# Kernel optimization log

Hardware: AMD Instinct MI355X
Metric: run time of the kernel (lower is better)

## Reference

```python
import jax, jax.numpy as jnp
import numpy as np

B, S, H = 32, 64, 512
ATT = 128


def _window_index_tables(seq_len):
    # Enumerate all contiguous windows of size 2..S, same set (order-independent
    # for the softmax-weighted sum) as the torch double loop.
    starts, ends = [], []
    for w in range(2, seq_len + 1):
        for s in range(0, seq_len - w + 1):
            starts.append(s)
            ends.append(s + w)
    starts = np.asarray(starts, np.int32)
    ends = np.asarray(ends, np.int32)
    widths = ends - starts
    ks = np.floor(np.log2(widths)).astype(np.int32)  # sparse-table level per window
    e2 = ends - (1 << ks)                            # second gather position
    return starts, e2, ks


def setup_inputs() -> dict:
    key = jax.random.key(0)
    k0, k1, k2, k3, k4 = jax.random.split(key, 5)
    return {
        "lstm_out": jax.random.normal(k0, (B, S, H), dtype=jnp.float32),
        "W1": jax.random.normal(k1, (H, ATT), dtype=jnp.float32) * 0.05,
        "b1": jax.random.normal(k2, (ATT,), dtype=jnp.float32) * 0.05,
        "W2": jax.random.normal(k3, (ATT, 1), dtype=jnp.float32) * 0.05,
        "b2": jax.random.normal(k4, (1,), dtype=jnp.float32) * 0.05,
    }


def reference(lstm_out, W1, b1, W2, b2):
    b, s, h = lstm_out.shape
    # Sparse table: M[k][:, i] = max over lstm_out[:, i : i+2^k] (clipped to s).
    n_levels = int(np.floor(np.log2(s))) + 1
    tables = [lstm_out]
    for k in range(1, n_levels):
        half = 1 << (k - 1)
        prev = tables[-1]
        shifted = jnp.concatenate(
            [prev[:, half:], jnp.full((b, half, h), -jnp.inf, prev.dtype)], axis=1)
        tables.append(jnp.maximum(prev, shifted))
    Mstack = jnp.stack(tables)  # [K, B, S, H]

    starts, e2, ks = _window_index_tables(s)
    # Range max of each window = max of two overlapping power-of-two blocks.
    pooled = jnp.maximum(Mstack[ks, :, starts], Mstack[ks, :, e2])  # [n_win, B, H]
    pooled = jnp.transpose(pooled, (1, 0, 2))  # [B, n_win, H]

    hid = jax.nn.relu(jnp.einsum("bnh,ha->bna", pooled, W1) + b1)
    scores = jnp.einsum("bna,ao->bno", hid, W2) + b2  # [B, n_win, 1]
    attn = jax.nn.softmax(scores, axis=1)
    return jnp.sum(attn * pooled, axis=1)  # [B, H]
```

## Files before the change

### kernel.cpp

```cpp
#include <hip/hip_runtime.h>
#include <stdint.h>


typedef unsigned short u16;
typedef unsigned int u32;

#define B_    32
#define S_    64
#define H_    512
#define ATT_  128
#define NWIN  2016
#define NLEV  7

typedef __bf16 bf16x8 __attribute__((ext_vector_type(8)));
typedef float  f32x4  __attribute__((ext_vector_type(4)));

__device__ __forceinline__ float asf(u32 i) {
  union { u32 i; float f; } v; v.i = i; return v.f;
}
__device__ __forceinline__ u32 asu(float f) {
  union { float f; u32 i; } v; v.f = f; return v.i;
}
__device__ __forceinline__ float bf2f(u16 u) { return asf(((u32)u) << 16); }
__device__ __forceinline__ u16 f2bf(float f) {
  u32 i = asu(f);
  i += 0x7fffu + ((i >> 16) & 1u);
  return (u16)(i >> 16);
}
__device__ __forceinline__ u32 bfmax2(u32 a, u32 b) {
  float a0 = asf(a << 16), a1 = asf(a & 0xffff0000u);
  float b0 = asf(b << 16), b1 = asf(b & 0xffff0000u);
  u32 m0 = asu(fmaxf(a0, b0)), m1 = asu(fmaxf(a1, b1));
  return (m1 & 0xffff0000u) | (m0 >> 16);
}
__device__ __forceinline__ uint4 bfmax8(uint4 a, uint4 b) {
  uint4 m;
  m.x = bfmax2(a.x, b.x); m.y = bfmax2(a.y, b.y);
  m.z = bfmax2(a.z, b.z); m.w = bfmax2(a.w, b.w);
  return m;
}
__device__ __forceinline__ bf16x8 as_bf16x8(uint4 v) {
  union { uint4 u; bf16x8 h; } c; c.u = v; return c.h;
}

__launch_bounds__(256)
__global__ void k01_init(const float* __restrict__ lstm, const float* __restrict__ W1,
                         u16* __restrict__ table, u16* __restrict__ w1t,
                         u16* __restrict__ widx) {
  int bid = blockIdx.x, tid = threadIdx.x;
  __shared__ u16 bufA[64 * 64], bufB[64 * 64];
  if (bid < 256) {
    int hc = bid & 7, b = bid >> 3;
    const float* src = lstm + (size_t)b * S_ * H_ + hc * 64;
    u16* tb = table + (size_t)b * NLEV * S_ * H_ + hc * 64;
    for (int t = tid; t < 64 * 16; t += 256) {
      int r = t >> 4, c4 = t & 15;
      float4 f = *reinterpret_cast<const float4*>(src + r * H_ + c4 * 4);
      ushort4 u;
      u.x = f2bf(f.x); u.y = f2bf(f.y); u.z = f2bf(f.z); u.w = f2bf(f.w);
      *reinterpret_cast<ushort4*>(&bufA[r * 64 + c4 * 4]) = u;
      *reinterpret_cast<ushort4*>(tb + r * H_ + c4 * 4) = u;
    }
    u16* pa = bufA; u16* pb = bufB;
    for (int k = 1; k < NLEV; ++k) {
      __syncthreads();
      int half = 1 << (k - 1);
      u16* dst_g = tb + k * S_ * H_;
      for (int t = tid; t < 64 * 16; t += 256) {
        int r = t >> 4, c4 = t & 15;
        int r2 = r + half; if (r2 > 63) r2 = 63;
        uint2 a  = *reinterpret_cast<const uint2*>(&pa[r  * 64 + c4 * 4]);
        uint2 bq = *reinterpret_cast<const uint2*>(&pa[r2 * 64 + c4 * 4]);
        uint2 m; m.x = bfmax2(a.x, bq.x); m.y = bfmax2(a.y, bq.y);
        *reinterpret_cast<uint2*>(&pb[r * 64 + c4 * 4]) = m;
        *reinterpret_cast<uint2*>(dst_g + r * H_ + c4 * 4) = m;
      }
      u16* tmp = pa; pa = pb; pb = tmp;
    }
  } else {
    int gb = bid - 256;
    if (gb == 0) {
      for (int n = tid; n < NWIN; n += 256) {
        int w = 2, rem = n;
        while (rem >= 65 - w) { rem -= 65 - w; ++w; }
        int s = rem;
        int k = 31 - __clz(w);
        int e2 = s + w - (1 << k);
        widx[n] = (u16)(s | (e2 << 6) | (k << 12));
      }
    }
    for (int q = tid; q < 2048; q += 256) {
      int idx = gb * 2048 + q;
      int n = idx >> 9, kq = idx & 511;
      w1t[idx] = f2bf(W1[kq * ATT_ + n]);
    }
  }
}

__launch_bounds__(256)
__attribute__((amdgpu_waves_per_eu(1, 4)))
__global__ void k2_scores(const u16* __restrict__ table, const u16* __restrict__ w1t,
                          const float* __restrict__ b1, const float* __restrict__ w2,
                          const u16* __restrict__ widx, float* __restrict__ scores) {
  const int b = blockIdx.y, mt = blockIdx.x;
  __shared__ u16 Ts[128 * 64];
  __shared__ u16 Bs[128 * 64];
  __shared__ u16 widx_l[96];
  __shared__ float b1s[128], w2s[128], sc[96];
  int tid = threadIdx.x;
  if (tid < 96) { widx_l[tid] = widx[mt * 96 + tid]; sc[tid] = 0.f; }
  if (tid < 128) { b1s[tid] = b1[tid]; w2s[tid] = w2[tid]; }
  __syncthreads();

  const int lv_lo = widx_l[0] >> 12;
  const u16* tb = table + (size_t)b * NLEV * S_ * H_ + (size_t)lv_lo * S_ * H_;

  int t0 = tid, t1 = tid + 256, t2 = tid + 512, t3 = tid + 768;
  int r0 = t0 >> 3, r1 = t1 >> 3, r2 = t2 >> 3, r3 = t3 >> 3;
  int c0 = t0 & 7,  c1 = t1 & 7,  c2 = t2 & 7,  c3 = t3 & 7;
  const u16* ts0 = tb + r0 * H_ + c0 * 8;
  const u16* ts1 = tb + r1 * H_ + c1 * 8;
  const u16* ts2 = tb + r2 * H_ + c2 * 8;
  const u16* ts3 = tb + r3 * H_ + c3 * 8;
  const u16* bs0 = w1t + r0 * H_ + c0 * 8;
  const u16* bs1 = w1t + r1 * H_ + c1 * 8;
  const u16* bs2 = w1t + r2 * H_ + c2 * 8;
  const u16* bs3 = w1t + r3 * H_ + c3 * 8;
  int sd0 = r0 * 64 + ((c0 ^ (r0 & 7)) * 8);
  int sd1 = r1 * 64 + ((c1 ^ (r1 & 7)) * 8);
  int sd2 = r2 * 64 + ((c2 ^ (r2 & 7)) * 8);
  int sd3 = r3 * 64 + ((c3 ^ (r3 & 7)) * 8);

  int wid = tid >> 6, lane = tid & 63;
  int wm = wid & 1, wn = wid >> 1;
  int lrow = lane & 15, quad = lane >> 4;

  int aoff[3][2][2];
#pragma unroll
  for (int i = 0; i < 3; ++i) {
    int m = wm * 48 + i * 16 + lrow;
    int pk = widx_l[m];
    int s = pk & 63, e2 = (pk >> 6) & 63, lv = (pk >> 12) - lv_lo;
    int rs = lv * 64 + s, re = lv * 64 + e2;
#pragma unroll
    for (int k2i = 0; k2i < 2; ++k2i) {
      int c = quad + k2i * 4;
      aoff[i][k2i][0] = rs * 64 + ((c ^ (rs & 7)) * 8);
      aoff[i][k2i][1] = re * 64 + ((c ^ (re & 7)) * 8);
    }
  }
  int boff[4][2];
#pragma unroll
  for (int j = 0; j < 4; ++j) {
    int n = wn * 64 + j * 16 + lrow;
#pragma unroll
    for (int k2i = 0; k2i < 2; ++k2i) {
      int c = quad + k2i * 4;
      boff[j][k2i] = n * 64 + ((c ^ (n & 7)) * 8);
    }
  }

  uint4 rT0, rT1, rT2, rT3, rB0, rB1, rB2, rB3;

#define ISSUE(KK) do { \
  rT0 = *reinterpret_cast<const uint4*>(ts0 + (KK)); \
  rT1 = *reinterpret_cast<const uint4*>(ts1 + (KK)); \
  rT2 = *reinterpret_cast<const uint4*>(ts2 + (KK)); \
  rT3 = *reinterpret_cast<const uint4*>(ts3 + (KK)); \
  rB0 = *reinterpret_cast<const uint4*>(bs0 + (KK)); \
  rB1 = *reinterpret_cast<const uint4*>(bs1 + (KK)); \
  rB2 = *reinterpret_cast<const uint4*>(bs2 + (KK)); \
  rB3 = *reinterpret_cast<const uint4*>(bs3 + (KK)); \
} while (0)

#define STAGE() do { \
  *reinterpret_cast<uint4*>(&Ts[sd0]) = rT0; \
  *reinterpret_cast<uint4*>(&Ts[sd1]) = rT1; \
  *reinterpret_cast<uint4*>(&Ts[sd2]) = rT2; \
  *reinterpret_cast<uint4*>(&Ts[sd3]) = rT3; \
  *reinterpret_cast<uint4*>(&Bs[sd0]) = rB0; \
  *reinterpret_cast<uint4*>(&Bs[sd1]) = rB1; \
  *reinterpret_cast<uint4*>(&Bs[sd2]) = rB2; \
  *reinterpret_cast<uint4*>(&Bs[sd3]) = rB3; \
} while (0)

#define MFMA_CHUNK() do { \
  _Pragma("unroll") for (int k2i = 0; k2i < 2; ++k2i) { \
    bf16x8 af[3], bfr[4]; \
    _Pragma("unroll") for (int i = 0; i < 3; ++i) { \
      uint4 va = *reinterpret_cast<const uint4*>(&Ts[aoff[i][k2i][0]]); \
      uint4 vb = *reinterpret_cast<const uint4*>(&Ts[aoff[i][k2i][1]]); \
      af[i] = as_bf16x8(bfmax8(va, vb)); } \
    _Pragma("unroll") for (int j = 0; j < 4; ++j) \
      bfr[j] = *reinterpret_cast<const bf16x8*>(&Bs[boff[j][k2i]]); \
    _Pragma("unroll") for (int i = 0; i < 3; ++i) \
      _Pragma("unroll") for (int j = 0; j < 4; ++j) \
        acc[i][j] = __builtin_amdgcn_mfma_f32_16x16x32_bf16(af[i], bfr[j], acc[i][j], 0, 0, 0); \
  } \
} while (0)

  ISSUE(0);

  f32x4 acc[3][4];
#pragma unroll
  for (int i = 0; i < 3; ++i)
#pragma unroll
    for (int j = 0; j < 4; ++j) acc[i][j] = (f32x4){0.f, 0.f, 0.f, 0.f};

  for (int kc = 0; kc < 7; ++kc) {
    __syncthreads();
    STAGE();
    __syncthreads();
    ISSUE((kc + 1) * 64);
    MFMA_CHUNK();
  }
  __syncthreads();
  STAGE();
  __syncthreads();
  MFMA_CHUNK();

#undef ISSUE
#undef STAGE
#undef MFMA_CHUNK

#pragma unroll
  for (int i = 0; i < 3; ++i) {
#pragma unroll
    for (int r = 0; r < 4; ++r) {
      float p = 0.f;
#pragma unroll
      for (int j = 0; j < 4; ++j) {
        int n = wn * 64 + j * 16 + lrow;
        float v = acc[i][j][r] + b1s[n];
        p += (v > 0.f ? v : 0.f) * w2s[n];
      }
      p += __shfl_xor(p, 1, 16);
      p += __shfl_xor(p, 2, 16);
      p += __shfl_xor(p, 4, 16);
      p += __shfl_xor(p, 8, 16);
      if (lrow == 0) atomicAdd(&sc[wm * 48 + i * 16 + quad * 4 + r], p);
    }
  }
  __syncthreads();
  if (tid < 96) scores[b * NWIN + mt * 96 + tid] = sc[tid];
}

__launch_bounds__(256)
__global__ void k34_out(const u16* __restrict__ table, const float* __restrict__ scores,
                        const u16* __restrict__ widx, float* __restrict__ out) {
  int hc = blockIdx.x, b = blockIdx.y, tid = threadIdx.x;
  __shared__ u16 Tl[6 * 64 * 32];
  __shared__ float attn_l[NWIN];
  __shared__ u16 widx_l[NWIN];
  __shared__ float red[8][32];
  __shared__ float wredM[4], wredS[4];
  const u16* tb = table + (size_t)b * NLEV * S_ * H_ + S_ * H_;
  int h0 = hc * 32;
  int lane = tid & 63, wid = tid >> 6;

  for (int t = tid; t < 6 * 64 * 4; t += 256) {
    int row = t >> 2, c = t & 3;
    uint4 v = *reinterpret_cast<const uint4*>(tb + row * H_ + h0 + c * 8);
    *reinterpret_cast<uint4*>(&Tl[row * 32 + c * 8]) = v;
  }
  for (int n = tid; n < NWIN; n += 256) widx_l[n] = widx[n];

  float mx = -1e30f;
  for (int n = tid; n < NWIN; n += 256) {
    float v = scores[b * NWIN + n];
    attn_l[n] = v;
    mx = fmaxf(mx, v);
  }
#pragma unroll
  for (int off = 32; off > 0; off >>= 1) mx = fmaxf(mx, __shfl_xor(mx, off, 64));
  if (lane == 0) wredM[wid] = mx;
  __syncthreads();
  mx = fmaxf(fmaxf(wredM[0], wredM[1]), fmaxf(wredM[2], wredM[3]));
  float sum = 0.f;
  for (int n = tid; n < NWIN; n += 256) {
    float e = __expf(attn_l[n] - mx);
    attn_l[n] = e;
    sum += e;
  }
#pragma unroll
  for (int off = 32; off > 0; off >>= 1) sum += __shfl_xor(sum, off, 64);
  if (lane == 0) wredS[wid] = sum;
  __syncthreads();
  float inv = 1.f / (wredS[0] + wredS[1] + wredS[2] + wredS[3]);

  int h = tid & 31, g = tid >> 5;
  float acc = 0.f;
  for (int n = g * 252; n < g * 252 + 252; ++n) {
    int pk = widx_l[n];
    int s = pk & 63, e2 = (pk >> 6) & 63, lv = pk >> 12;
    float va = bf2f(Tl[((lv - 1) * 64 + s) * 32 + h]);
    float vb = bf2f(Tl[((lv - 1) * 64 + e2) * 32 + h]);
    acc += attn_l[n] * fmaxf(va, vb);
  }
  red[g][h] = acc;
  __syncthreads();
  if (tid < 32) {
    float s2 = 0.f;
#pragma unroll
    for (int g2 = 0; g2 < 8; ++g2) s2 += red[g2][tid];
    out[b * H_ + h0 + tid] = s2 * inv;
  }
}

extern "C" void kernel_launch(void* const* d_in, const int* in_sizes, int n_in,
                              void* d_out, int out_size, void* d_ws, size_t ws_size,
                              hipStream_t stream) {
  const float* lstm = (const float*)d_in[0];
  const float* W1   = (const float*)d_in[1];
  const float* b1   = (const float*)d_in[2];
  const float* W2   = (const float*)d_in[3];
  float* out = (float*)d_out;

  char* ws = (char*)d_ws;
  u16*   widx   = (u16*)(ws + 0);
  u16*   w1t    = (u16*)(ws + 4096);
  u16*   table  = (u16*)(ws + 135168);
  float* scores = (float*)(ws + 14815232);

  k01_init <<<288, 256, 0, stream>>>(lstm, W1, table, w1t, widx);
  k2_scores<<<dim3(21, B_), 256, 0, stream>>>(table, w1t, b1, W2, widx, scores);
  k34_out  <<<dim3(16, B_), 256, 0, stream>>>(table, scores, widx, out);
}
```

Before: 123.8 us.

## Retile score GEMM to 64-window tiles and drop unused level-0 table

The score kernel now gives each block 64 windows instead of 96. Each wave handles 16 windows across all 128 attention columns, so the shared-memory atomic reduction is gone and scores are written directly. The grid grows from 21 to 32 tiles per batch, and the last tile is partially masked. The sparse table no longer stores level 0, since windows start at width 2. This saves global writes and workspace, and all table indexing is shifted by one level. The cost is that each block still stages the same full 128-row tile for fewer windows, so the redundant staged loads grow.

Measured after the change: 116.6 us. 1.06x faster.

```diff
diff --git a/kernel.cpp b/kernel.cpp
--- a/kernel.cpp
+++ b/kernel.cpp
@@ -11,6 +11,7 @@
 #define ATT_  128
 #define NWIN  2016
 #define NLEV  7
+#define TLEV  6
 
 typedef __bf16 bf16x8 __attribute__((ext_vector_type(8)));
 typedef float  f32x4  __attribute__((ext_vector_type(4)));
@@ -52,20 +53,19 @@
   if (bid < 256) {
     int hc = bid & 7, b = bid >> 3;
     const float* src = lstm + (size_t)b * S_ * H_ + hc * 64;
-    u16* tb = table + (size_t)b * NLEV * S_ * H_ + hc * 64;
+    u16* tb = table + (size_t)b * TLEV * S_ * H_ + hc * 64;
     for (int t = tid; t < 64 * 16; t += 256) {
       int r = t >> 4, c4 = t & 15;
       float4 f = *reinterpret_cast<const float4*>(src + r * H_ + c4 * 4);
       ushort4 u;
       u.x = f2bf(f.x); u.y = f2bf(f.y); u.z = f2bf(f.z); u.w = f2bf(f.w);
       *reinterpret_cast<ushort4*>(&bufA[r * 64 + c4 * 4]) = u;
-      *reinterpret_cast<ushort4*>(tb + r * H_ + c4 * 4) = u;
     }
     u16* pa = bufA; u16* pb = bufB;
     for (int k = 1; k < NLEV; ++k) {
       __syncthreads();
       int half = 1 << (k - 1);
-      u16* dst_g = tb + k * S_ * H_;
+      u16* dst_g = tb + (size_t)(k - 1) * S_ * H_;
       for (int t = tid; t < 64 * 16; t += 256) {
         int r = t >> 4, c4 = t & 15;
         int r2 = r + half; if (r2 > 63) r2 = 63;
@@ -105,15 +105,18 @@
   const int b = blockIdx.y, mt = blockIdx.x;
   __shared__ u16 Ts[128 * 64];
   __shared__ u16 Bs[128 * 64];
-  __shared__ u16 widx_l[96];
-  __shared__ float b1s[128], w2s[128], sc[96];
+  __shared__ u16 widx_l[64];
+  __shared__ float b1s[128], w2s[128];
   int tid = threadIdx.x;
-  if (tid < 96) { widx_l[tid] = widx[mt * 96 + tid]; sc[tid] = 0.f; }
+  if (tid < 64) {
+    int n = mt * 64 + tid; if (n > NWIN - 1) n = NWIN - 1;
+    widx_l[tid] = widx[n];
+  }
   if (tid < 128) { b1s[tid] = b1[tid]; w2s[tid] = w2[tid]; }
   __syncthreads();
 
   const int lv_lo = widx_l[0] >> 12;
-  const u16* tb = table + (size_t)b * NLEV * S_ * H_ + (size_t)lv_lo * S_ * H_;
+  const u16* tb = table + (size_t)b * TLEV * S_ * H_ + (size_t)(lv_lo - 1) * S_ * H_;
 
   int t0 = tid, t1 = tid + 256, t2 = tid + 512, t3 = tid + 768;
   int r0 = t0 >> 3, r1 = t1 >> 3, r2 = t2 >> 3, r3 = t3 >> 3;
@@ -132,27 +135,24 @@
   int sd3 = r3 * 64 + ((c3 ^ (r3 & 7)) * 8);
 
   int wid = tid >> 6, lane = tid & 63;
-  int wm = wid & 1, wn = wid >> 1;
   int lrow = lane & 15, quad = lane >> 4;
 
-  int aoff[3][2][2];
-#pragma unroll
-  for (int i = 0; i < 3; ++i) {
-    int m = wm * 48 + i * 16 + lrow;
-    int pk = widx_l[m];
+  int aoff[2][2];
+  {
+    int pk = widx_l[wid * 16 + lrow];
     int s = pk & 63, e2 = (pk >> 6) & 63, lv = (pk >> 12) - lv_lo;
     int rs = lv * 64 + s, re = lv * 64 + e2;
 #pragma unroll
     for (int k2i = 0; k2i < 2; ++k2i) {
       int c = quad + k2i * 4;
-      aoff[i][k2i][0] = rs * 64 + ((c ^ (rs & 7)) * 8);
-      aoff[i][k2i][1] = re * 64 + ((c ^ (re & 7)) * 8);
-    }
-  }
-  int boff[4][2];
-#pragma unroll
-  for (int j = 0; j < 4; ++j) {
-    int n = wn * 64 + j * 16 + lrow;
+      aoff[k2i][0] = rs * 64 + ((c ^ (rs & 7)) * 8);
+      aoff[k2i][1] = re * 64 + ((c ^ (re & 7)) * 8);
+    }
+  }
+  int boff[8][2];
+#pragma unroll
+  for (int j = 0; j < 8; ++j) {
+    int n = j * 16 + lrow;
 #pragma unroll
     for (int k2i = 0; k2i < 2; ++k2i) {
       int c = quad + k2i * 4;
@@ -184,65 +184,65 @@
   *reinterpret_cast<uint4*>(&Bs[sd3]) = rB3; \
 } while (0)
 
-#define MFMA_CHUNK() do { \
-  _Pragma("unroll") for (int k2i = 0; k2i < 2; ++k2i) { \
-    bf16x8 af[3], bfr[4]; \
-    _Pragma("unroll") for (int i = 0; i < 3; ++i) { \
-      uint4 va = *reinterpret_cast<const uint4*>(&Ts[aoff[i][k2i][0]]); \
-      uint4 vb = *reinterpret_cast<const uint4*>(&Ts[aoff[i][k2i][1]]); \
-      af[i] = as_bf16x8(bfmax8(va, vb)); } \
-    _Pragma("unroll") for (int j = 0; j < 4; ++j) \
-      bfr[j] = *reinterpret_cast<const bf16x8*>(&Bs[boff[j][k2i]]); \
-    _Pragma("unroll") for (int i = 0; i < 3; ++i) \
-      _Pragma("unroll") for (int j = 0; j < 4; ++j) \
-        acc[i][j] = __builtin_amdgcn_mfma_f32_16x16x32_bf16(af[i], bfr[j], acc[i][j], 0, 0, 0); \
-  } \
-} while (0)
-
   ISSUE(0);
 
-  f32x4 acc[3][4];
-#pragma unroll
-  for (int i = 0; i < 3; ++i)
-#pragma unroll
-    for (int j = 0; j < 4; ++j) acc[i][j] = (f32x4){0.f, 0.f, 0.f, 0.f};
+  f32x4 acc[8];
+#pragma unroll
+  for (int j = 0; j < 8; ++j) acc[j] = (f32x4){0.f, 0.f, 0.f, 0.f};
 
   for (int kc = 0; kc < 7; ++kc) {
     __syncthreads();
     STAGE();
     __syncthreads();
     ISSUE((kc + 1) * 64);
-    MFMA_CHUNK();
+#pragma unroll
+    for (int k2i = 0; k2i < 2; ++k2i) {
+      uint4 va = *reinterpret_cast<const uint4*>(&Ts[aoff[k2i][0]]);
+      uint4 vb = *reinterpret_cast<const uint4*>(&Ts[aoff[k2i][1]]);
+      bf16x8 af = as_bf16x8(bfmax8(va, vb));
+#pragma unroll
+      for (int j = 0; j < 8; ++j) {
+        bf16x8 bfr = *reinterpret_cast<const bf16x8*>(&Bs[boff[j][k2i]]);
+        acc[j] = __builtin_amdgcn_mfma_f32_16x16x32_bf16(af, bfr, acc[j], 0, 0, 0);
+      }
+    }
   }
   __syncthreads();
   STAGE();
   __syncthreads();
-  MFMA_CHUNK();
+#pragma unroll
+  for (int k2i = 0; k2i < 2; ++k2i) {
+    uint4 va = *reinterpret_cast<const uint4*>(&Ts[aoff[k2i][0]]);
+    uint4 vb = *reinterpret_cast<const uint4*>(&Ts[aoff[k2i][1]]);
+    bf16x8 af = as_bf16x8(bfmax8(va, vb));
+#pragma unroll
+    for (int j = 0; j < 8; ++j) {
+      bf16x8 bfr = *reinterpret_cast<const bf16x8*>(&Bs[boff[j][k2i]]);
+      acc[j] = __builtin_amdgcn_mfma_f32_16x16x32_bf16(af, bfr, acc[j], 0, 0, 0);
+    }
+  }
 
 #undef ISSUE
 #undef STAGE
-#undef MFMA_CHUNK
-
-#pragma unroll
-  for (int i = 0; i < 3; ++i) {
-#pragma unroll
-    for (int r = 0; r < 4; ++r) {
-      float p = 0.f;
-#pragma unroll
-      for (int j = 0; j < 4; ++j) {
-        int n = wn * 64 + j * 16 + lrow;
-        float v = acc[i][j][r] + b1s[n];
-        p += (v > 0.f ? v : 0.f) * w2s[n];
-      }
-      p += __shfl_xor(p, 1, 16);
-      p += __shfl_xor(p, 2, 16);
-      p += __shfl_xor(p, 4, 16);
-      p += __shfl_xor(p, 8, 16);
-      if (lrow == 0) atomicAdd(&sc[wm * 48 + i * 16 + quad * 4 + r], p);
-    }
-  }
-  __syncthreads();
-  if (tid < 96) scores[b * NWIN + mt * 96 + tid] = sc[tid];
+
+#pragma unroll
+  for (int r = 0; r < 4; ++r) {
+    float p = 0.f;
+#pragma unroll
+    for (int j = 0; j < 8; ++j) {
+      int n = j * 16 + lrow;
+      float v = acc[j][r] + b1s[n];
+      p += (v > 0.f ? v : 0.f) * w2s[n];
+    }
+    p += __shfl_xor(p, 1, 16);
+    p += __shfl_xor(p, 2, 16);
+    p += __shfl_xor(p, 4, 16);
+    p += __shfl_xor(p, 8, 16);
+    if (lrow == 0) {
+      int nw = mt * 64 + wid * 16 + quad * 4 + r;
+      if (nw < NWIN) scores[b * NWIN + nw] = p;
+    }
+  }
 }
 
 __launch_bounds__(256)
@@ -254,7 +254,7 @@
   __shared__ u16 widx_l[NWIN];
   __shared__ float red[8][32];
   __shared__ float wredM[4], wredS[4];
-  const u16* tb = table + (size_t)b * NLEV * S_ * H_ + S_ * H_;
+  const u16* tb = table + (size_t)b * TLEV * S_ * H_;
   int h0 = hc * 32;
   int lane = tid & 63, wid = tid >> 6;
 
@@ -320,9 +320,9 @@
   u16*   widx   = (u16*)(ws + 0);
   u16*   w1t    = (u16*)(ws + 4096);
   u16*   table  = (u16*)(ws + 135168);
-  float* scores = (float*)(ws + 14815232);
+  float* scores = (float*)(ws + 12718080);
 
   k01_init <<<288, 256, 0, stream>>>(lstm, W1, table, w1t, widx);
-  k2_scores<<<dim3(21, B_), 256, 0, stream>>>(table, w1t, b1, W2, widx, scores);
+  k2_scores<<<dim3(32, B_), 256, 0, stream>>>(table, w1t, b1, W2, widx, scores);
   k34_out  <<<dim3(16, B_), 256, 0, stream>>>(table, scores, widx, out);
 }
```
